# Optimization experiments

Hardware: AMD Instinct MI355X
Metric: run time of the kernel (lower is better)

Reference implementation:

```python
import jax, jax.numpy as jnp
import numpy as np

T = 0.07          # temperature (params[1])
B, N, D, C = 128, 100000, 128, 40  # batch, bank size (outputSize=K), feat dim (inputSize-1), n classes
STDV = 1.0 / np.sqrt((D + 1) / 3.0)  # init scale from __init__


def setup_inputs() -> dict:
    key = jax.random.key(0)
    k1, k2, k3, k4, k5, k6 = jax.random.split(key, 6)
    x = jax.random.normal(k1, (B, D), dtype=jnp.float32)
    x = x / jnp.linalg.norm(x, axis=1, keepdims=True)  # unit-norm features (keeps exp(out/T) in range)
    y = jax.random.randint(k2, (B,), 0, N)
    labels = jax.random.randint(k3, (B,), 0, C)
    bank_labels = jax.random.randint(k4, (N,), 0, C).astype(jnp.float32)
    mem_feats = (jax.random.uniform(k5, (N, D), dtype=jnp.float32) * 2.0 - 1.0) * STDV
    da_feats = (jax.random.uniform(k6, (N, D), dtype=jnp.float32) * 2.0 - 1.0) * STDV
    memory = jnp.concatenate([bank_labels[:, None], mem_feats], axis=1)      # [N, 1+D], col 0 = label
    memory_da = jnp.concatenate([bank_labels[:, None], da_feats], axis=1)    # [N, 1+D], col 0 = label
    return {"x": x, "y": y, "labels": labels, "memory_da": memory_da, "memory": memory}


def reference(x, y, labels, memory_da, memory):
    # NCEFunction.forward: out[b,n] = exp(x[b] . memory_da[n,1:] / T), Z-normalized per row (Z<0 branch)
    n_out = memory_da.shape[0]
    feats = memory_da[:, 1:]                               # [N, D] gathered features
    out = jnp.exp(jnp.einsum('bd,nd->bn', x, feats) / T)   # [B, N] (torch bmm over repeated bank)
    Z1 = out.mean(axis=1, keepdims=True) * n_out           # per-row Z estimate
    out = out / Z1
    # idx: per-label torch.where loop -> expressed densely as a boolean match matrix [B, N]
    idx_mask = memory_da[None, :, 0] == labels[:, None].astype(memory_da.dtype)
    return out, idx_mask
```

## Files before the change

kernel.cpp:

```cpp
#include <hip/hip_runtime.h>
#include <hip/hip_bf16.h>

#define NB 128
#define NMEM 100000
#define ND 128
constexpr float T_INV = 1.0f / 0.07f;

constexpr int LROW = ND + 8;
constexpr int NTW = NMEM / 16;
constexpr int GRID = 512;
constexpr int NWAVES = GRID * 4;
constexpr int ZSTRIDE = 16;

typedef __attribute__((ext_vector_type(8))) __bf16 bf16x8;
typedef __attribute__((ext_vector_type(4))) float f32x4;
struct bf4 { __bf16 a, b, c, d; };

template<bool PASS2>
__global__ __launch_bounds__(256, 2) void nce_wave(
    const float* __restrict__ x,
    const int* __restrict__ labels,
    const float* __restrict__ mem_da,
    float* __restrict__ zbuf,
    float* __restrict__ out,
    float* __restrict__ maskout)
{
  __shared__ __bf16 xs[NB * LROW];
  __shared__ float aux[NB];
  __shared__ float zl[NB];

  const int tid = threadIdx.x;

  const float4* x4 = (const float4*)x;
  float4 xv[16];
  #pragma unroll
  for (int i = 0; i < 16; ++i) xv[i] = x4[tid + i * 256];
  #pragma unroll
  for (int i = 0; i < 16; ++i) {
    int g4 = tid + i * 256;
    *(bf4*)&xs[(g4 >> 5) * LROW + (g4 & 31) * 4] =
        bf4{(__bf16)xv[i].x, (__bf16)xv[i].y, (__bf16)xv[i].z, (__bf16)xv[i].w};
  }
  if (tid < NB) {
    if (PASS2) aux[tid] = 1.0f / zbuf[tid * ZSTRIDE];
    else { aux[tid] = (float)labels[tid]; zl[tid] = 0.f; }
  }
  __syncthreads();

  const int wid = tid >> 6, lane = tid & 63, q = lane >> 4, l16 = lane & 15;
  const int wgid = blockIdx.x * 4 + wid;

  f32x4 am[8];
  #pragma unroll
  for (int mt = 0; mt < 8; ++mt) am[mt] = *(const f32x4*)&aux[mt * 16 + q * 4];

  f32x4 zacc[8];
  #pragma unroll
  for (int mt = 0; mt < 8; ++mt) zacc[mt] = (f32x4){0.f, 0.f, 0.f, 0.f};

  for (int t = wgid; t < NTW; t += NWAVES) {
    const float* rowp = mem_da + (size_t)(t * 16 + l16) * 129;
    float ln;
    if (!PASS2) ln = rowp[0];
    float bf[4][8];
    #pragma unroll
    for (int kc = 0; kc < 4; ++kc)
      __builtin_memcpy(&bf[kc][0], rowp + 1 + kc * 32 + q * 8, 32);
    bf16x8 bb[4];
    #pragma unroll
    for (int kc = 0; kc < 4; ++kc)
      #pragma unroll
      for (int j = 0; j < 8; ++j) bb[kc][j] = (__bf16)bf[kc][j];

    f32x4 acc[8];
    #pragma unroll
    for (int mt = 0; mt < 8; ++mt) acc[mt] = (f32x4){0.f, 0.f, 0.f, 0.f};
    #pragma unroll
    for (int kc = 0; kc < 4; ++kc) {
      const int ko = kc * 32 + q * 8;
      #pragma unroll
      for (int mt = 0; mt < 8; ++mt) {
        bf16x8 a = *(const bf16x8*)&xs[(mt * 16 + l16) * LROW + ko];
        acc[mt] = __builtin_amdgcn_mfma_f32_16x16x32_bf16(a, bb[kc], acc[mt], 0, 0, 0);
      }
    }

    const size_t n = (size_t)t * 16 + l16;
    #pragma unroll
    for (int mt = 0; mt < 8; ++mt) {
      #pragma unroll
      for (int r = 0; r < 4; ++r) {
        const size_t off = (size_t)(mt * 16 + q * 4 + r) * NMEM + n;
        if (!PASS2) {
          zacc[mt][r] += __expf(acc[mt][r] * T_INV);
          maskout[off] = (ln == am[mt][r]) ? 1.0f : 0.0f;
        } else {
          out[off] = __expf(acc[mt][r] * T_INV) * am[mt][r];
        }
      }
    }
  }

  if (!PASS2) {
    #pragma unroll
    for (int mt = 0; mt < 8; ++mt) {
      #pragma unroll
      for (int r = 0; r < 4; ++r) {
        float v = zacc[mt][r];
        v += __shfl_xor(v, 1);
        v += __shfl_xor(v, 2);
        v += __shfl_xor(v, 4);
        v += __shfl_xor(v, 8);
        if (l16 == 0) atomicAdd(&zl[mt * 16 + q * 4 + r], v);
      }
    }
    __syncthreads();
    if (tid < NB) atomicAdd(&zbuf[tid * ZSTRIDE], zl[tid]);
  }
}

extern "C" void kernel_launch(void* const* d_in, const int* in_sizes, int n_in,
                              void* d_out, int out_size, void* d_ws, size_t ws_size,
                              hipStream_t stream) {
  const float* x      = (const float*)d_in[0];
  const int* labels   = (const int*)d_in[2];
  const float* mem_da = (const float*)d_in[3];
  float* out     = (float*)d_out;
  float* maskout = out + (size_t)NB * NMEM;
  float* zbuf    = (float*)d_ws;

  hipMemsetAsync(zbuf, 0, NB * ZSTRIDE * sizeof(float), stream);
  nce_wave<false><<<GRID, 256, 0, stream>>>(x, labels, mem_da, zbuf, nullptr, maskout);
  nce_wave<true ><<<GRID, 256, 0, stream>>>(x, labels, mem_da, zbuf, out, nullptr);
}
```

Before: 204.8 us.

## Swap MFMA operands for vectorized row stores and fold normalization into exp2

The MFMA operand order is swapped so that each lane holds four consecutive bank columns of one batch row. This lets the output and mask writes become 16-byte vector stores instead of scalar strided stores. Each wave now processes two 16-row bank tiles per iteration, and bank labels are broadcast via shuffles. The exponent uses exp2 with a prescaled constant, and the 1/Z division is folded in as an added -log2(Z) term. The Z reduction shuffles across quads instead of within 16-lane groups.

```diff
diff --git a/kernel.cpp b/kernel.cpp
--- a/kernel.cpp
+++ b/kernel.cpp
@@ -4,10 +4,10 @@
 #define NB 128
 #define NMEM 100000
 #define ND 128
-constexpr float T_INV = 1.0f / 0.07f;
+constexpr float K2 = 20.6099442241331655f;
 
 constexpr int LROW = ND + 8;
-constexpr int NTW = NMEM / 16;
+constexpr int NTP = NMEM / 32;
 constexpr int GRID = 512;
 constexpr int NWAVES = GRID * 4;
 constexpr int ZSTRIDE = 16;
@@ -42,7 +42,7 @@
         bf4{(__bf16)xv[i].x, (__bf16)xv[i].y, (__bf16)xv[i].z, (__bf16)xv[i].w};
   }
   if (tid < NB) {
-    if (PASS2) aux[tid] = 1.0f / zbuf[tid * ZSTRIDE];
+    if (PASS2) aux[tid] = -__log2f(zbuf[tid * ZSTRIDE]);
     else { aux[tid] = (float)labels[tid]; zl[tid] = 0.f; }
   }
   __syncthreads();
@@ -50,52 +50,69 @@
   const int wid = tid >> 6, lane = tid & 63, q = lane >> 4, l16 = lane & 15;
   const int wgid = blockIdx.x * 4 + wid;
 
-  f32x4 am[8];
+  float lblb[8];
   #pragma unroll
-  for (int mt = 0; mt < 8; ++mt) am[mt] = *(const f32x4*)&aux[mt * 16 + q * 4];
+  for (int mt = 0; mt < 8; ++mt) lblb[mt] = aux[mt * 16 + l16];
 
-  f32x4 zacc[8];
+  float zacc[8];
   #pragma unroll
-  for (int mt = 0; mt < 8; ++mt) zacc[mt] = (f32x4){0.f, 0.f, 0.f, 0.f};
+  for (int mt = 0; mt < 8; ++mt) zacc[mt] = 0.f;
 
-  for (int t = wgid; t < NTW; t += NWAVES) {
-    const float* rowp = mem_da + (size_t)(t * 16 + l16) * 129;
-    float ln;
-    if (!PASS2) ln = rowp[0];
-    float bf[4][8];
+  for (int t = wgid; t < NTP; t += NWAVES) {
     #pragma unroll
-    for (int kc = 0; kc < 4; ++kc)
-      __builtin_memcpy(&bf[kc][0], rowp + 1 + kc * 32 + q * 8, 32);
-    bf16x8 bb[4];
-    #pragma unroll
-    for (int kc = 0; kc < 4; ++kc)
+    for (int h = 0; h < 2; ++h) {
+      const int n0 = t * 32 + h * 16;
+      const float* rowp = mem_da + (size_t)(n0 + l16) * 129;
+      float ln;
+      if (!PASS2) ln = rowp[0];
+
+      bf16x8 ab[4];
       #pragma unroll
-      for (int j = 0; j < 8; ++j) bb[kc][j] = (__bf16)bf[kc][j];
+      for (int kc = 0; kc < 4; ++kc) {
+        float tmp[8];
+        __builtin_memcpy(tmp, rowp + 1 + kc * 32 + q * 8, 32);
+        #pragma unroll
+        for (int j = 0; j < 8; ++j) ab[kc][j] = (__bf16)tmp[j];
+      }
 
-    f32x4 acc[8];
-    #pragma unroll
-    for (int mt = 0; mt < 8; ++mt) acc[mt] = (f32x4){0.f, 0.f, 0.f, 0.f};
-    #pragma unroll
-    for (int kc = 0; kc < 4; ++kc) {
-      const int ko = kc * 32 + q * 8;
+      f32x4 acc[8];
+      #pragma unroll
+      for (int mt = 0; mt < 8; ++mt) acc[mt] = (f32x4){0.f, 0.f, 0.f, 0.f};
+      #pragma unroll
+      for (int kc = 0; kc < 4; ++kc) {
+        const int ko = kc * 32 + q * 8;
+        #pragma unroll
+        for (int mt = 0; mt < 8; ++mt) {
+          bf16x8 xb = *(const bf16x8*)&xs[(mt * 16 + l16) * LROW + ko];
+          acc[mt] = __builtin_amdgcn_mfma_f32_16x16x32_bf16(ab[kc], xb, acc[mt], 0, 0, 0);
+        }
+      }
+
+      float ml[4];
+      if (!PASS2) {
+        #pragma unroll
+        for (int r = 0; r < 4; ++r) ml[r] = __shfl(ln, q * 4 + r, 16);
+      }
+
       #pragma unroll
       for (int mt = 0; mt < 8; ++mt) {
-        bf16x8 a = *(const bf16x8*)&xs[(mt * 16 + l16) * LROW + ko];
-        acc[mt] = __builtin_amdgcn_mfma_f32_16x16x32_bf16(a, bb[kc], acc[mt], 0, 0, 0);
-      }
-    }
-
-    const size_t n = (size_t)t * 16 + l16;
-    #pragma unroll
-    for (int mt = 0; mt < 8; ++mt) {
-      #pragma unroll
-      for (int r = 0; r < 4; ++r) {
-        const size_t off = (size_t)(mt * 16 + q * 4 + r) * NMEM + n;
+        const size_t off = (size_t)(mt * 16 + l16) * NMEM + n0 + q * 4;
         if (!PASS2) {
-          zacc[mt][r] += __expf(acc[mt][r] * T_INV);
-          maskout[off] = (ln == am[mt][r]) ? 1.0f : 0.0f;
+          f32x4 mk;
+          float zs = 0.f;
+          #pragma unroll
+          for (int r = 0; r < 4; ++r) {
+            zs += exp2f(acc[mt][r] * K2);
+            mk[r] = (ml[r] == lblb[mt]) ? 1.0f : 0.0f;
+          }
+          zacc[mt] += zs;
+          *(f32x4*)&maskout[off] = mk;
         } else {
-          out[off] = __expf(acc[mt][r] * T_INV) * am[mt][r];
+          f32x4 ov;
+          #pragma unroll
+          for (int r = 0; r < 4; ++r)
+            ov[r] = exp2f(__builtin_fmaf(acc[mt][r], K2, lblb[mt]));
+          *(f32x4*)&out[off] = ov;
         }
       }
     }
@@ -104,15 +121,10 @@
   if (!PASS2) {
     #pragma unroll
     for (int mt = 0; mt < 8; ++mt) {
-      #pragma unroll
-      for (int r = 0; r < 4; ++r) {
-        float v = zacc[mt][r];
-        v += __shfl_xor(v, 1);
-        v += __shfl_xor(v, 2);
-        v += __shfl_xor(v, 4);
-        v += __shfl_xor(v, 8);
-        if (l16 == 0) atomicAdd(&zl[mt * 16 + q * 4 + r], v);
-      }
+      float v = zacc[mt];
+      v += __shfl_xor(v, 16);
+      v += __shfl_xor(v, 32);
+      if (lane < 16) atomicAdd(&zl[mt * 16 + lane], v);
     }
     __syncthreads();
     if (tid < NB) atomicAdd(&zbuf[tid * ZSTRIDE], zl[tid]);
```

New measurement: 279.3 us. 1.36x slower.
